# Kernel tuning notes

Hardware: AMD Instinct MI355X
Metric: run time of the kernel (lower is better)

## Reference

```python
import jax, jax.numpy as jnp
import numpy as np

B, FH, N, TIN = 8, 8, 2048, 5      # batch(time for LSTM), f_length, nodes, in_length
H1, H2 = 32, 64                    # traj_linear_hidden, lstm_encoder_size
NEG = -9e15

def setup_inputs() -> dict:
    key = jax.random.key(0)
    ks = jax.random.split(key, 12)
    s = lambda k, shape, fan: jax.random.normal(k, shape, jnp.float32) * (1.0 / np.sqrt(fan))
    return {
        "hist": jax.random.normal(ks[0], (B, FH, N, TIN), jnp.float32),
        "adj": jax.random.randint(ks[1], (B, 2, N, N), 0, 2, jnp.int32),
        "W1": s(ks[2], (H1, TIN * FH), TIN * FH),
        "b1": jnp.zeros((H1,), jnp.float32),
        "W_ih": s(ks[3], (4 * H2, H1), H1),
        "W_hh": s(ks[4], (4 * H2, H2), H2),
        "b_ih": jnp.zeros((4 * H2,), jnp.float32),
        "b_hh": jnp.zeros((4 * H2,), jnp.float32),
        "Wg": s(ks[5], (H2, H2), H2),
        "a_src": s(ks[6], (H2,), H2),
        "a_dst": s(ks[7], (H2,), H2),
    }

def _lstm(x, W_ih, W_hh, b_ih, b_hh):
    # x: [T, Nb, H1] (torch nn.LSTM seq-first); gate order i,f,g,o
    Nb = x.shape[1]
    h0 = jnp.zeros((Nb, H2), x.dtype)
    c0 = jnp.zeros((Nb, H2), x.dtype)
    def step(carry, xt):
        h, c = carry
        g = xt @ W_ih.T + b_ih + h @ W_hh.T + b_hh        # [Nb, 4*H2]
        i, f, gg, o = jnp.split(g, 4, axis=-1)
        c = jax.nn.sigmoid(f) * c + jax.nn.sigmoid(i) * jnp.tanh(gg)
        h = jax.nn.sigmoid(o) * jnp.tanh(c)
        return (h, c), h
    _, hs = jax.lax.scan(step, (h0, c0), x)
    return hs                                              # [T, Nb, H2]

def reference(hist, adj, W1, b1, W_ih, W_hh, b_ih, b_hh, Wg, a_src, a_dst):
    # hist.permute(0,2,3,1).flatten(2,3) -> [B, N, TIN*FH]
    x = jnp.transpose(hist, (0, 2, 3, 1)).reshape(B, N, TIN * FH)
    h1 = jax.nn.elu(x @ W1.T + b1)                         # [B, N, H1]
    hs = _lstm(h1, W_ih, W_hh, b_ih, b_hh)                 # [B, N, H2]
    # GAT over adj[:, -1]
    A = adj[:, -1, :, :] > 0                               # [B, N, N]
    Wh = hs @ Wg                                           # [B, N, H2]
    e = jax.nn.leaky_relu(
        (Wh @ a_src)[:, :, None] + (Wh @ a_dst)[:, None, :], 0.2)
    e = jnp.where(A, e, NEG)
    alpha = jax.nn.softmax(e, axis=-1)                     # [B, N, N]
    out = jax.nn.elu(jnp.einsum("bij,bjd->bid", alpha, Wh))
    return out
```

## Files before the change

kernel.cpp:

```cpp
#include <hip/hip_runtime.h>
#include <hip/hip_bf16.h>
#include <math.h>

#define BB 8
#define FH 8
#define NN 2048
#define TIN 5
#define H1 32
#define H2 64

typedef const void* cvp;
typedef __attribute__((ext_vector_type(8))) short short8;
typedef __attribute__((ext_vector_type(4))) float floatx4;

__device__ __forceinline__ float ldx(cvp p, int i, int bf) {
  if (bf) return __bfloat162float(((const __hip_bfloat16*)p)[i]);
  return ((const float*)p)[i];
}

__device__ __forceinline__ float4 ld4(cvp p, int i, int bf) {
  if (bf) {
    const __hip_bfloat162* q = (const __hip_bfloat162*)p;
    float2 a = __bfloat1622float2(q[(i >> 1)]);
    float2 b = __bfloat1622float2(q[(i >> 1) + 1]);
    return make_float4(a.x, a.y, b.x, b.y);
  }
  return ((const float4*)p)[i >> 2];
}

__device__ __forceinline__ float sigf(float x) {
  return __fdividef(1.f, 1.f + __expf(-x));
}
__device__ __forceinline__ float tanhfast(float x) {
  float e = __expf(x + x);
  return 1.f - __fdividef(2.f, e + 1.f);
}

__device__ __forceinline__ int detect_bf(cvp wih) {
  unsigned word = ((const unsigned*)wih)[threadIdx.x & 63];
  unsigned e = (word >> 7) & 0xFFu;
  unsigned long long bal = __ballot(e >= 100u && e <= 150u);
  return __popcll(bal) > 44;
}

__global__ __launch_bounds__(256, 2) void k_lstm(
    cvp hist, cvp W1, cvp b1, cvp W_ih, cvp W_hh, cvp b_ih, cvp b_hh,
    cvp Wg, cvp a_src, cvp a_dst, const int* __restrict__ adj,
    __hip_bfloat16* __restrict__ WhFr, float* __restrict__ sv,
    float* __restrict__ dv, unsigned* __restrict__ gmask) {
  __shared__ __align__(16) float xh[4][96];
  __shared__ float gbuf[4][256];
  __shared__ float W1s[H1][41];
  __shared__ float b1s[H1];
  __shared__ float xstage[2][4][40];
  __shared__ __align__(16) unsigned pmsk[2048];

  int bf = detect_bf(W_ih);
  int tid = threadIdx.x;
  int w = tid >> 6, lane = tid & 63;
  int g = tid;
  int n0 = blockIdx.x << 2;
  int node_w = n0 + w;

  int cb = blockIdx.x >> 6;
  int ci = (blockIdx.x & 63) << 5;
  const int4* adj4 = (const int4*)(adj + ((size_t)(cb * 2 + 1) * NN + ci) * NN);

  for (int i = tid; i < H1 * 40; i += 256) W1s[i / 40][i % 40] = ldx(W1, i, bf);
  if (tid < H1) b1s[tid] = ldx(b1, tid, bf);
  for (int i = tid; i < 2048; i += 256) pmsk[i] = 0u;
  int snd = tid / 40, sr = tid % 40;
  int sti = sr >> 3, sf = sr & 7;
  if (tid < 160)
    xstage[0][snd][sr] = ldx(hist, ((0 * FH + sf) * NN + n0 + snd) * TIN + sti, bf);
  xh[w][32 + lane] = 0.f;

  float wreg[96];
#pragma unroll
  for (int kq = 0; kq < 8; ++kq) {
    float4 v = ld4(W_ih, g * 32 + (kq << 2), bf);
    wreg[(kq << 2) + 0] = v.x; wreg[(kq << 2) + 1] = v.y;
    wreg[(kq << 2) + 2] = v.z; wreg[(kq << 2) + 3] = v.w;
  }
#pragma unroll
  for (int kq = 0; kq < 16; ++kq) {
    float4 v = ld4(W_hh, g * 64 + (kq << 2), bf);
    wreg[32 + (kq << 2) + 0] = v.x; wreg[32 + (kq << 2) + 1] = v.y;
    wreg[32 + (kq << 2) + 2] = v.z; wreg[32 + (kq << 2) + 3] = v.w;
  }
  float bias = ldx(b_ih, g, bf) + ldx(b_hh, g, bf);

  float wgreg[64];
#pragma unroll
  for (int k = 0; k < H2; ++k) wgreg[k] = ldx(Wg, (k << 6) + lane, bf);
  float as = ldx(a_src, lane, bf);
  float ad = ldx(a_dst, lane, bf);

  size_t o8base = ((size_t)(node_w >> 5) * 256) + ((size_t)(lane >> 4) * 64) +
                  (((node_w >> 3) & 3) * 16) + (lane & 15);
  int jj = node_w & 7;

  float c = 0.f;

  for (int t = 0; t < BB; ++t) {
    float hv = 0.f;
    if (t < 7 && tid < 160)
      hv = ldx(hist, (((t + 1) * FH + sf) * NN + n0 + snd) * TIN + sti, bf);
    int4 av0[4];
#pragma unroll
    for (int u = 0; u < 4; ++u) av0[u] = adj4[(t << 11) + (u << 8) + tid];
    __syncthreads();
    if (tid < 128) {
      int nd = tid >> 5, k = tid & 31;
      float acc = b1s[k];
#pragma unroll
      for (int j = 0; j < 40; ++j) acc += W1s[k][j] * xstage[t & 1][nd][j];
      xh[nd][k] = (acc > 0.f) ? acc : expm1f(acc);
    }
    __syncthreads();
    float acc[4] = {bias, bias, bias, bias};
    const float4* xq0 = (const float4*)xh[0];
    const float4* xq1 = (const float4*)xh[1];
    const float4* xq2 = (const float4*)xh[2];
    const float4* xq3 = (const float4*)xh[3];
#pragma unroll
    for (int kq = 0; kq < 24; ++kq) {
      float w0 = wreg[(kq << 2) + 0], w1 = wreg[(kq << 2) + 1];
      float w2 = wreg[(kq << 2) + 2], w3 = wreg[(kq << 2) + 3];
      float4 v0 = xq0[kq], v1 = xq1[kq], v2 = xq2[kq], v3 = xq3[kq];
      acc[0] += w0 * v0.x + w1 * v0.y + w2 * v0.z + w3 * v0.w;
      acc[1] += w0 * v1.x + w1 * v1.y + w2 * v1.z + w3 * v1.w;
      acc[2] += w0 * v2.x + w1 * v2.y + w2 * v2.z + w3 * v2.w;
      acc[3] += w0 * v3.x + w1 * v3.y + w2 * v3.z + w3 * v3.w;
    }
#pragma unroll
    for (int nd = 0; nd < 4; ++nd) gbuf[nd][g] = acc[nd];
#pragma unroll
    for (int u = 0; u < 4; ++u) {
      int gg = (t << 11) + (u << 8) + tid;
      unsigned nib = (av0[u].x != 0 ? 1u : 0u) | (av0[u].y != 0 ? 2u : 0u) |
                     (av0[u].z != 0 ? 4u : 0u) | (av0[u].w != 0 ? 8u : 0u);
      atomicOr(&pmsk[((gg >> 9) << 6) + ((gg & 511) >> 3)],
               nib << ((gg & 7) << 2));
    }
    int4 av1[4];
#pragma unroll
    for (int u = 0; u < 4; ++u) av1[u] = adj4[(t << 11) + ((u + 4) << 8) + tid];
    __syncthreads();
    float gi = gbuf[w][lane];
    float gf = gbuf[w][64 + lane];
    float gg0 = gbuf[w][128 + lane];
    float go = gbuf[w][192 + lane];
    c = sigf(gf) * c + sigf(gi) * tanhfast(gg0);
    float h = sigf(go) * tanhfast(c);
    xh[w][32 + lane] = h;

    float wh = 0.f;
    const float4* hq = (const float4*)&xh[w][32];
#pragma unroll
    for (int kq = 0; kq < 16; ++kq) {
      float4 hvv = hq[kq];
      wh += hvv.x * wgreg[(kq << 2) + 0] + hvv.y * wgreg[(kq << 2) + 1] +
            hvv.z * wgreg[(kq << 2) + 2] + hvv.w * wgreg[(kq << 2) + 3];
    }
    float s = wh * as, d = wh * ad;
#pragma unroll
    for (int off = 32; off > 0; off >>= 1) {
      s += __shfl_xor(s, off, 64);
      d += __shfl_xor(d, off, 64);
    }
    if (lane == 0) {
      sv[t * NN + node_w] = s;
      dv[t * NN + node_w] = d;
    }
    WhFr[((size_t)t * 16384 + o8base) * 8 + jj] = __float2bfloat16(wh);

    if (t < 7 && tid < 160) xstage[(t + 1) & 1][snd][sr] = hv;
#pragma unroll
    for (int u = 0; u < 4; ++u) {
      int gg2 = (t << 11) + ((u + 4) << 8) + tid;
      unsigned nib = (av1[u].x != 0 ? 1u : 0u) | (av1[u].y != 0 ? 2u : 0u) |
                     (av1[u].z != 0 ? 4u : 0u) | (av1[u].w != 0 ? 8u : 0u);
      atomicOr(&pmsk[((gg2 >> 9) << 6) + ((gg2 & 511) >> 3)],
               nib << ((gg2 & 7) << 2));
    }
    __syncthreads();
  }
  const int4* ps = (const int4*)pmsk;
  int4* gm4 = (int4*)gmask + ((size_t)blockIdx.x << 9);
  gm4[tid] = ps[tid];
  gm4[256 + tid] = ps[256 + tid];
}

__global__ __launch_bounds__(256, 4) void k_gat(
    const unsigned* __restrict__ gmask, const __hip_bfloat16* __restrict__ WhFr,
    const float* __restrict__ sv, const float* __restrict__ dv,
    void* __restrict__ out, cvp W_ih) {
  __shared__ __align__(16) float dv_s[NN];
  __shared__ unsigned int msk[16 * 65];
  __shared__ floatx4 abuf[3][5][64];
  int bf = detect_bf(W_ih);
  int tid = threadIdx.x;
  int w = tid >> 6, lane = tid & 63;
  int b = blockIdx.x >> 7;
  int i0 = (blockIdx.x & 127) << 4;
  int q = lane >> 4, m = lane & 15;

  const int4* gm4 = (const int4*)gmask + (((size_t)b * NN + i0) << 4);
  int4 mv = gm4[tid];
  {
    int mrow = tid >> 4, mwd = (tid & 15) << 2;
    unsigned* mp = &msk[mrow * 65 + mwd];
    mp[0] = (unsigned)mv.x; mp[1] = (unsigned)mv.y;
    mp[2] = (unsigned)mv.z; mp[3] = (unsigned)mv.w;
  }
  {
    const float4* dsrc = (const float4*)(dv + (size_t)b * NN);
    ((float4*)dv_s)[tid] = dsrc[tid];
    ((float4*)dv_s)[256 + tid] = dsrc[256 + tid];
  }
  float sva = sv[b * NN + i0 + m];
  __syncthreads();

  short8 ones;
#pragma unroll
  for (int p = 0; p < 8; ++p) ones[p] = (short)0x3F80;

  const short8* base = ((const short8*)WhFr) + (size_t)b * 16384 + lane;
  int ksb = w << 4, kse = ksb + 16;
  floatx4 acc0 = {0.f, 0.f, 0.f, 0.f};
  floatx4 acc1 = acc0, acc2 = acc0, acc3 = acc0, accS = acc0;

  for (int ks = ksb; ks < kse; ++ks) {
    const short8* b_ks = base + (size_t)ks * 256;
    short8 b0 = b_ks[0];
    short8 b1 = b_ks[64];
    short8 b2 = b_ks[128];
    short8 b3 = b_ks[192];
    unsigned mword = msk[m * 65 + ks];
    float4 d0 = *(const float4*)&dv_s[(ks << 5) + (q << 3)];
    float4 d1 = *(const float4*)&dv_s[(ks << 5) + (q << 3) + 4];
    float dd[8] = {d0.x, d0.y, d0.z, d0.w, d1.x, d1.y, d1.z, d1.w};
    float pv[8];
#pragma unroll
    for (int jj = 0; jj < 8; ++jj) {
      float t = sva + dd[jj];
      float e = __expf(fmaxf(t, 0.2f * t));
      pv[jj] = ((mword >> ((q << 3) + jj)) & 1u) ? e : 0.f;
    }
    short8 afr;
#pragma unroll
    for (int p2 = 0; p2 < 4; ++p2)
      ((__hip_bfloat162*)&afr)[p2] =
          __float22bfloat162_rn(make_float2(pv[2 * p2], pv[2 * p2 + 1]));
    acc0 = __builtin_amdgcn_mfma_f32_16x16x32_bf16(afr, b0, acc0, 0, 0, 0);
    acc1 = __builtin_amdgcn_mfma_f32_16x16x32_bf16(afr, b1, acc1, 0, 0, 0);
    acc2 = __builtin_amdgcn_mfma_f32_16x16x32_bf16(afr, b2, acc2, 0, 0, 0);
    acc3 = __builtin_amdgcn_mfma_f32_16x16x32_bf16(afr, b3, acc3, 0, 0, 0);
    accS = __builtin_amdgcn_mfma_f32_16x16x32_bf16(afr, ones, accS, 0, 0, 0);
  }
  if (w > 0) {
    abuf[w - 1][0][lane] = acc0;
    abuf[w - 1][1][lane] = acc1;
    abuf[w - 1][2][lane] = acc2;
    abuf[w - 1][3][lane] = acc3;
    abuf[w - 1][4][lane] = accS;
  }
  __syncthreads();
  if (w != 0) return;
#pragma unroll
  for (int ww = 0; ww < 3; ++ww) {
    acc0 += abuf[ww][0][lane];
    acc1 += abuf[ww][1][lane];
    acc2 += abuf[ww][2][lane];
    acc3 += abuf[ww][3][lane];
    accS += abuf[ww][4][lane];
  }
  floatx4 accs[4] = {acc0, acc1, acc2, acc3};
  float inv[4];
#pragma unroll
  for (int r = 0; r < 4; ++r) inv[r] = 1.f / accS[r];
  if (bf) {
    __hip_bfloat16* o = (__hip_bfloat16*)out;
#pragma unroll
    for (int nt = 0; nt < 4; ++nt)
#pragma unroll
      for (int r = 0; r < 4; ++r) {
        float v = accs[nt][r] * inv[r];
        v = (v > 0.f) ? v : expm1f(v);
        int row = i0 + (q << 2) + r;
        o[((size_t)b * NN + row) * H2 + (nt << 4) + m] = __float2bfloat16(v);
      }
  } else {
    float* o = (float*)out;
#pragma unroll
    for (int nt = 0; nt < 4; ++nt)
#pragma unroll
      for (int r = 0; r < 4; ++r) {
        float v = accs[nt][r] * inv[r];
        v = (v > 0.f) ? v : expm1f(v);
        int row = i0 + (q << 2) + r;
        o[((size_t)b * NN + row) * H2 + (nt << 4) + m] = v;
      }
  }
}

extern "C" void kernel_launch(void* const* d_in, const int* in_sizes, int n_in,
                              void* d_out, int out_size, void* d_ws, size_t ws_size,
                              hipStream_t stream) {
  (void)in_sizes; (void)n_in; (void)out_size; (void)ws_size;
  cvp hist  = d_in[0];
  const int* adj = (const int*)d_in[1];
  cvp W1    = d_in[2];
  cvp b1    = d_in[3];
  cvp W_ih  = d_in[4];
  cvp W_hh  = d_in[5];
  cvp b_ih  = d_in[6];
  cvp b_hh  = d_in[7];
  cvp Wg    = d_in[8];
  cvp a_src = d_in[9];
  cvp a_dst = d_in[10];

  float* ws = (float*)d_ws;
  __hip_bfloat16* WhFr = (__hip_bfloat16*)d_ws;
  float* sv = ws + 524288;
  float* dv = sv + BB * NN;
  unsigned* gmask = (unsigned*)(dv + BB * NN);

  k_lstm<<<512, 256, 0, stream>>>(hist, W1, b1, W_ih, W_hh, b_ih, b_hh,
                                  Wg, a_src, a_dst, adj, WhFr, sv, dv, gmask);
  k_gat<<<1024, 256, 0, stream>>>(gmask, WhFr, sv, dv, d_out, W_ih);
}
```

Baseline: 383.8 us.

## Process two 16-row tiles per GAT block to reuse Wh fragments, prefetch next k-step

Each k_gat block now handles 32 query rows instead of 16, so every loaded Wh B-fragment feeds two sets of MFMAs, and the grid is halved to 512 blocks. The Wh fragments for the next k-step are software-prefetched into registers. This aims to halve global reads of Wh and hide load latency, at the cost of doubling accumulator registers (launch bounds drop to 2 blocks per CU), more exp work per thread, and an extra reduction pass through shared memory.

Result: no change. 386.0 us (+0.6%).

```diff
diff --git a/kernel.cpp b/kernel.cpp
--- a/kernel.cpp
+++ b/kernel.cpp
@@ -192,24 +192,26 @@
   gm4[256 + tid] = ps[256 + tid];
 }
 
-__global__ __launch_bounds__(256, 4) void k_gat(
+__global__ __launch_bounds__(256, 2) void k_gat(
     const unsigned* __restrict__ gmask, const __hip_bfloat16* __restrict__ WhFr,
     const float* __restrict__ sv, const float* __restrict__ dv,
     void* __restrict__ out, cvp W_ih) {
   __shared__ __align__(16) float dv_s[NN];
-  __shared__ unsigned int msk[16 * 65];
+  __shared__ unsigned int msk[32 * 65];
   __shared__ floatx4 abuf[3][5][64];
   int bf = detect_bf(W_ih);
   int tid = threadIdx.x;
   int w = tid >> 6, lane = tid & 63;
-  int b = blockIdx.x >> 7;
-  int i0 = (blockIdx.x & 127) << 4;
+  int b = blockIdx.x >> 6;
+  int i0 = (blockIdx.x & 63) << 5;
   int q = lane >> 4, m = lane & 15;
 
   const int4* gm4 = (const int4*)gmask + (((size_t)b * NN + i0) << 4);
-  int4 mv = gm4[tid];
-  {
-    int mrow = tid >> 4, mwd = (tid & 15) << 2;
+#pragma unroll
+  for (int u = 0; u < 2; ++u) {
+    int idx = (u << 8) + tid;
+    int4 mv = gm4[idx];
+    int mrow = idx >> 4, mwd = (idx & 15) << 2;
     unsigned* mp = &msk[mrow * 65 + mwd];
     mp[0] = (unsigned)mv.x; mp[1] = (unsigned)mv.y;
     mp[2] = (unsigned)mv.z; mp[3] = (unsigned)mv.w;
@@ -219,7 +221,8 @@
     ((float4*)dv_s)[tid] = dsrc[tid];
     ((float4*)dv_s)[256 + tid] = dsrc[256 + tid];
   }
-  float sva = sv[b * NN + i0 + m];
+  float sva0 = sv[b * NN + i0 + m];
+  float sva1 = sv[b * NN + i0 + 16 + m];
   __syncthreads();
 
   short8 ones;
@@ -228,80 +231,107 @@
 
   const short8* base = ((const short8*)WhFr) + (size_t)b * 16384 + lane;
   int ksb = w << 4, kse = ksb + 16;
-  floatx4 acc0 = {0.f, 0.f, 0.f, 0.f};
-  floatx4 acc1 = acc0, acc2 = acc0, acc3 = acc0, accS = acc0;
+  floatx4 z = {0.f, 0.f, 0.f, 0.f};
+  floatx4 a0a = z, a1a = z, a2a = z, a3a = z, aSa = z;
+  floatx4 a0b = z, a1b = z, a2b = z, a3b = z, aSb = z;
+
+  const short8* bp = base + (size_t)ksb * 256;
+  short8 nb0 = bp[0], nb1 = bp[64], nb2 = bp[128], nb3 = bp[192];
 
   for (int ks = ksb; ks < kse; ++ks) {
-    const short8* b_ks = base + (size_t)ks * 256;
-    short8 b0 = b_ks[0];
-    short8 b1 = b_ks[64];
-    short8 b2 = b_ks[128];
-    short8 b3 = b_ks[192];
-    unsigned mword = msk[m * 65 + ks];
+    short8 b0 = nb0, b1 = nb1, b2 = nb2, b3 = nb3;
+    if (ks + 1 < kse) {
+      const short8* np = base + (size_t)(ks + 1) * 256;
+      nb0 = np[0]; nb1 = np[64]; nb2 = np[128]; nb3 = np[192];
+    }
+    unsigned mw0 = msk[m * 65 + ks];
+    unsigned mw1 = msk[(16 + m) * 65 + ks];
     float4 d0 = *(const float4*)&dv_s[(ks << 5) + (q << 3)];
     float4 d1 = *(const float4*)&dv_s[(ks << 5) + (q << 3) + 4];
     float dd[8] = {d0.x, d0.y, d0.z, d0.w, d1.x, d1.y, d1.z, d1.w};
-    float pv[8];
+    float pv0[8], pv1[8];
 #pragma unroll
     for (int jj = 0; jj < 8; ++jj) {
-      float t = sva + dd[jj];
-      float e = __expf(fmaxf(t, 0.2f * t));
-      pv[jj] = ((mword >> ((q << 3) + jj)) & 1u) ? e : 0.f;
-    }
-    short8 afr;
-#pragma unroll
-    for (int p2 = 0; p2 < 4; ++p2)
-      ((__hip_bfloat162*)&afr)[p2] =
-          __float22bfloat162_rn(make_float2(pv[2 * p2], pv[2 * p2 + 1]));
-    acc0 = __builtin_amdgcn_mfma_f32_16x16x32_bf16(afr, b0, acc0, 0, 0, 0);
-    acc1 = __builtin_amdgcn_mfma_f32_16x16x32_bf16(afr, b1, acc1, 0, 0, 0);
-    acc2 = __builtin_amdgcn_mfma_f32_16x16x32_bf16(afr, b2, acc2, 0, 0, 0);
-    acc3 = __builtin_amdgcn_mfma_f32_16x16x32_bf16(afr, b3, acc3, 0, 0, 0);
-    accS = __builtin_amdgcn_mfma_f32_16x16x32_bf16(afr, ones, accS, 0, 0, 0);
-  }
-  if (w > 0) {
-    abuf[w - 1][0][lane] = acc0;
-    abuf[w - 1][1][lane] = acc1;
-    abuf[w - 1][2][lane] = acc2;
-    abuf[w - 1][3][lane] = acc3;
-    abuf[w - 1][4][lane] = accS;
-  }
-  __syncthreads();
-  if (w != 0) return;
-#pragma unroll
-  for (int ww = 0; ww < 3; ++ww) {
-    acc0 += abuf[ww][0][lane];
-    acc1 += abuf[ww][1][lane];
-    acc2 += abuf[ww][2][lane];
-    acc3 += abuf[ww][3][lane];
-    accS += abuf[ww][4][lane];
-  }
-  floatx4 accs[4] = {acc0, acc1, acc2, acc3};
-  float inv[4];
-#pragma unroll
-  for (int r = 0; r < 4; ++r) inv[r] = 1.f / accS[r];
-  if (bf) {
-    __hip_bfloat16* o = (__hip_bfloat16*)out;
-#pragma unroll
-    for (int nt = 0; nt < 4; ++nt)
-#pragma unroll
-      for (int r = 0; r < 4; ++r) {
-        float v = accs[nt][r] * inv[r];
-        v = (v > 0.f) ? v : expm1f(v);
-        int row = i0 + (q << 2) + r;
-        o[((size_t)b * NN + row) * H2 + (nt << 4) + m] = __float2bfloat16(v);
+      float t0 = sva0 + dd[jj];
+      float e0 = __expf(fmaxf(t0, 0.2f * t0));
+      pv0[jj] = ((mw0 >> ((q << 3) + jj)) & 1u) ? e0 : 0.f;
+      float t1 = sva1 + dd[jj];
+      float e1 = __expf(fmaxf(t1, 0.2f * t1));
+      pv1[jj] = ((mw1 >> ((q << 3) + jj)) & 1u) ? e1 : 0.f;
+    }
+    short8 afr0, afr1;
+#pragma unroll
+    for (int p2 = 0; p2 < 4; ++p2) {
+      ((__hip_bfloat162*)&afr0)[p2] =
+          __float22bfloat162_rn(make_float2(pv0[2 * p2], pv0[2 * p2 + 1]));
+      ((__hip_bfloat162*)&afr1)[p2] =
+          __float22bfloat162_rn(make_float2(pv1[2 * p2], pv1[2 * p2 + 1]));
+    }
+    a0a = __builtin_amdgcn_mfma_f32_16x16x32_bf16(afr0, b0, a0a, 0, 0, 0);
+    a1a = __builtin_amdgcn_mfma_f32_16x16x32_bf16(afr0, b1, a1a, 0, 0, 0);
+    a2a = __builtin_amdgcn_mfma_f32_16x16x32_bf16(afr0, b2, a2a, 0, 0, 0);
+    a3a = __builtin_amdgcn_mfma_f32_16x16x32_bf16(afr0, b3, a3a, 0, 0, 0);
+    aSa = __builtin_amdgcn_mfma_f32_16x16x32_bf16(afr0, ones, aSa, 0, 0, 0);
+    a0b = __builtin_amdgcn_mfma_f32_16x16x32_bf16(afr1, b0, a0b, 0, 0, 0);
+    a1b = __builtin_amdgcn_mfma_f32_16x16x32_bf16(afr1, b1, a1b, 0, 0, 0);
+    a2b = __builtin_amdgcn_mfma_f32_16x16x32_bf16(afr1, b2, a2b, 0, 0, 0);
+    a3b = __builtin_amdgcn_mfma_f32_16x16x32_bf16(afr1, b3, a3b, 0, 0, 0);
+    aSb = __builtin_amdgcn_mfma_f32_16x16x32_bf16(afr1, ones, aSb, 0, 0, 0);
+  }
+
+#pragma unroll
+  for (int tile = 0; tile < 2; ++tile) {
+    floatx4 c0 = tile ? a0b : a0a;
+    floatx4 c1 = tile ? a1b : a1a;
+    floatx4 c2 = tile ? a2b : a2a;
+    floatx4 c3 = tile ? a3b : a3a;
+    floatx4 cS = tile ? aSb : aSa;
+    if (w > 0) {
+      abuf[w - 1][0][lane] = c0;
+      abuf[w - 1][1][lane] = c1;
+      abuf[w - 1][2][lane] = c2;
+      abuf[w - 1][3][lane] = c3;
+      abuf[w - 1][4][lane] = cS;
+    }
+    __syncthreads();
+    if (w == 0) {
+#pragma unroll
+      for (int ww = 0; ww < 3; ++ww) {
+        c0 += abuf[ww][0][lane];
+        c1 += abuf[ww][1][lane];
+        c2 += abuf[ww][2][lane];
+        c3 += abuf[ww][3][lane];
+        cS += abuf[ww][4][lane];
       }
-  } else {
-    float* o = (float*)out;
-#pragma unroll
-    for (int nt = 0; nt < 4; ++nt)
-#pragma unroll
-      for (int r = 0; r < 4; ++r) {
-        float v = accs[nt][r] * inv[r];
-        v = (v > 0.f) ? v : expm1f(v);
-        int row = i0 + (q << 2) + r;
-        o[((size_t)b * NN + row) * H2 + (nt << 4) + m] = v;
+      floatx4 accs[4] = {c0, c1, c2, c3};
+      float inv[4];
+#pragma unroll
+      for (int r = 0; r < 4; ++r) inv[r] = 1.f / cS[r];
+      int rbase = i0 + (tile << 4) + (q << 2);
+      if (bf) {
+        __hip_bfloat16* o = (__hip_bfloat16*)out;
+#pragma unroll
+        for (int nt = 0; nt < 4; ++nt)
+#pragma unroll
+          for (int r = 0; r < 4; ++r) {
+            float v = accs[nt][r] * inv[r];
+            v = (v > 0.f) ? v : expm1f(v);
+            o[((size_t)b * NN + rbase + r) * H2 + (nt << 4) + m] =
+                __float2bfloat16(v);
+          }
+      } else {
+        float* o = (float*)out;
+#pragma unroll
+        for (int nt = 0; nt < 4; ++nt)
+#pragma unroll
+          for (int r = 0; r < 4; ++r) {
+            float v = accs[nt][r] * inv[r];
+            v = (v > 0.f) ? v : expm1f(v);
+            o[((size_t)b * NN + rbase + r) * H2 + (nt << 4) + m] = v;
+          }
       }
+    }
+    __syncthreads();
   }
 }
 
@@ -329,5 +359,5 @@
 
   k_lstm<<<512, 256, 0, stream>>>(hist, W1, b1, W_ih, W_hh, b_ih, b_hh,
                                   Wg, a_src, a_dst, adj, WhFr, sv, dv, gmask);
-  k_gat<<<1024, 256, 0, stream>>>(gmask, WhFr, sv, dv, d_out, W_ih);
-}
+  k_gat<<<512, 256, 0, stream>>>(gmask, WhFr, sv, dv, d_out, W_ih);
+}
```
